# Kernel optimization log

Hardware: AMD Instinct MI355X
Metric: run time of the kernel (lower is better)

The kernel has to match this reference:

```python
import jax, jax.numpy as jnp
import numpy as np

B, T, D_MODEL = 2, 1024, 1024
H, DEPTH = 8, 5
DH = D_MODEL // H


def setup_inputs() -> dict:
    key = jax.random.key(0)
    k_x, k_wp, k_bp, k_wv, k_wo = jax.random.split(key, 5)
    x = jax.random.normal(k_x, (B, T, D_MODEL), dtype=jnp.float32)
    # Parameters stored as [in, out] (y = x @ W + b), equivalent math to nn.Linear.
    Wp = jax.random.normal(k_wp, (D_MODEL, H * DEPTH), dtype=jnp.float32) * 0.02
    bp = jnp.zeros((H * DEPTH,), dtype=jnp.float32)
    Wv = jax.random.normal(k_wv, (D_MODEL, D_MODEL), dtype=jnp.float32) * 0.02
    Wo = jax.random.normal(k_wo, (D_MODEL, D_MODEL), dtype=jnp.float32) * 0.02
    return {"x": x, "Wp": Wp, "bp": bp, "Wv": Wv, "Wo": Wo}


def reference(x, Wp, bp, Wv, Wo):
    Bx, Tx, d = x.shape
    # soft binary path decisions: B,H,T,DEPTH
    paths = jax.nn.sigmoid(x @ Wp + bp)              # B,T,H*DEPTH
    paths = paths.reshape(Bx, Tx, H, DEPTH).transpose(0, 2, 1, 3)  # B,H,T,DEPTH
    # pairwise per-level agreement: B,H,Tq,Tk,DEPTH
    pq = paths[:, :, :, None, :]
    pk = paths[:, :, None, :, :]
    agree = pq * pk + (1.0 - pq) * (1.0 - pk)
    # shared-prefix length via cumprod over depth, summed
    sim = jnp.cumprod(agree, axis=-1).sum(axis=-1) / DEPTH  # B,H,Tq,Tk
    # causal mask
    mask = jnp.triu(jnp.ones((Tx, Tx), dtype=bool), k=1)
    sim = jnp.where(mask[None, None], -jnp.inf, sim)
    attn = jax.nn.softmax(sim, axis=-1)              # B,H,T,T
    V = (x @ Wv).reshape(Bx, Tx, H, DH).transpose(0, 2, 1, 3)  # B,H,T,dh
    ctx = jnp.einsum('bhqk,bhkd->bhqd', attn, V)
    ctx = ctx.transpose(0, 2, 1, 3).reshape(Bx, Tx, d)
    return ctx @ Wo
```

## Files before the change

### kernel.cpp

```cpp
#include <hip/hip_runtime.h>
#include <hip/hip_bf16.h>

#define B_ 2
#define T_ 1024
#define D_ 1024
#define H_ 8
#define DEPTH_ 5
#define DH_ 128

typedef short s16x8 __attribute__((ext_vector_type(8)));
typedef short s16x4 __attribute__((ext_vector_type(4)));
typedef float f32x4 __attribute__((ext_vector_type(4)));

__device__ inline short f2bf(float f) {
  __hip_bfloat16 h = __float2bfloat16(f);
  return *reinterpret_cast<short*>(&h);
}

#define MFMA16(a, b, c) __builtin_amdgcn_mfma_f32_16x16x32_bf16(a, b, c, 0, 0, 0)

typedef __attribute__((address_space(3))) unsigned int lds_u32_t;
typedef __attribute__((address_space(1))) unsigned int glb_u32_t;
__device__ __forceinline__ void glds16(const void* g, void* l) {
  __builtin_amdgcn_global_load_lds((const glb_u32_t*)g, (lds_u32_t*)l, 16, 0,
                                   0);
}

__global__ __launch_bounds__(256) void prep_kernel(
    const float* __restrict__ Wv, const float* __restrict__ Wo,
    const float* __restrict__ Wp, const float* __restrict__ x,
    short* __restrict__ WBt, short* __restrict__ Wot,
    short* __restrict__ xb) {
  int tid = threadIdx.x;
  if (blockIdx.z < 2) {
    const float* W = blockIdx.z ? Wo : Wv;
    short* Wt = blockIdx.z ? Wot : WBt;
    __shared__ float tile[64][65];
    int k0 = blockIdx.y * 64, n0 = blockIdx.x * 64;
#pragma unroll
    for (int i = 0; i < 4; ++i) {
      int idx = tid + i * 256;
      int r = idx >> 4, c4 = (idx & 15) * 4;
      float4 v = *(const float4*)&W[(size_t)(k0 + r) * D_ + n0 + c4];
      tile[r][c4 + 0] = v.x;
      tile[r][c4 + 1] = v.y;
      tile[r][c4 + 2] = v.z;
      tile[r][c4 + 3] = v.w;
    }
    __syncthreads();
#pragma unroll
    for (int j = 0; j < 2; ++j) {
      int idx = tid + j * 256;
      int n = idx >> 3, k8 = (idx & 7) * 8;
      s16x8 outv;
#pragma unroll
      for (int jj = 0; jj < 8; ++jj) outv[jj] = f2bf(tile[k8 + jj][n]);
      *(s16x8*)&Wt[(size_t)(n0 + n) * D_ + k0 + k8] = outv;
    }
  } else {
    int bid = blockIdx.y * 16 + blockIdx.x;
#pragma unroll
    for (int c = 0; c < 4; ++c) {
      size_t idx = (size_t)bid * 8192 + c * 2048 + tid * 8;
      float4 f0 = *(const float4*)&x[idx];
      float4 f1 = *(const float4*)&x[idx + 4];
      s16x8 v;
      v[0] = f2bf(f0.x); v[1] = f2bf(f0.y);
      v[2] = f2bf(f0.z); v[3] = f2bf(f0.w);
      v[4] = f2bf(f1.x); v[5] = f2bf(f1.y);
      v[6] = f2bf(f1.z); v[7] = f2bf(f1.w);
      *(s16x8*)&xb[idx] = v;
    }
    if (bid < 4) {
#pragma unroll
      for (int it = 0; it < 8; ++it) {
        int item = bid * 2048 + it * 256 + tid;
        int row = item >> 7, k8 = (item & 127) * 8;
        s16x8 v;
        if (row < H_ * DEPTH_) {
#pragma unroll
          for (int j = 0; j < 8; ++j)
            v[j] = f2bf(Wp[(size_t)(k8 + j) * (H_ * DEPTH_) + row]);
        } else {
#pragma unroll
          for (int j = 0; j < 8; ++j) v[j] = 0;
        }
        *(s16x8*)&WBt[(size_t)(1024 + row) * D_ + k8] = v;
      }
    }
  }
}

template <int MODE>
__global__ __launch_bounds__(256) void gemm128(
    const short* __restrict__ A, const short* __restrict__ Bt,
    float* __restrict__ Cf, short* __restrict__ Vt,
    const float* __restrict__ bp, float* __restrict__ paths_t) {
  __shared__ short As[64 * 128];
  __shared__ short Bs[64 * 128];
  const int K = D_;
  int tid = threadIdx.x;
  int bm = blockIdx.y << 6, bn = blockIdx.x << 6;
  int w = tid >> 6, lane = tid & 63;
  int wm = (w >> 1) * 32, wn = (w & 1) * 32;
  int g = lane >> 4, fr = lane & 15;
  f32x4 acc[2][2] = {{{0.f, 0.f, 0.f, 0.f}, {0.f, 0.f, 0.f, 0.f}},
                     {{0.f, 0.f, 0.f, 0.f}, {0.f, 0.f, 0.f, 0.f}}};

  int r4 = lane >> 4;
  int cg = lane & 15;
  const short* Asrc[4];
  const short* Bsrc[4];
  short* Adst[4];
  short* Bdst[4];
#pragma unroll
  for (int i = 0; i < 4; ++i) {
    int row = w * 16 + i * 4 + r4;
    int scol = (cg ^ (row & 15)) * 8;
    Asrc[i] = A + (size_t)(bm + row) * K + scol;
    Bsrc[i] = Bt + (size_t)(bn + row) * K + scol;
    Adst[i] = &As[(w * 16 + i * 4) * 128];
    Bdst[i] = &Bs[(w * 16 + i * 4) * 128];
  }

  for (int k0 = 0; k0 < K; k0 += 128) {
    __syncthreads();
#pragma unroll
    for (int i = 0; i < 4; ++i) {
      glds16(Asrc[i] + k0, Adst[i]);
      glds16(Bsrc[i] + k0, Bdst[i]);
    }
    __syncthreads();
#pragma unroll
    for (int ks = 0; ks < 4; ++ks) {
      int p = ((ks * 4 + g) ^ fr) * 8;
      s16x8 a0 = *(const s16x8*)&As[(wm + fr) * 128 + p];
      s16x8 a1 = *(const s16x8*)&As[(wm + 16 + fr) * 128 + p];
      s16x8 b0 = *(const s16x8*)&Bs[(wn + fr) * 128 + p];
      s16x8 b1 = *(const s16x8*)&Bs[(wn + 16 + fr) * 128 + p];
      acc[0][0] = MFMA16(a0, b0, acc[0][0]);
      acc[0][1] = MFMA16(a0, b1, acc[0][1]);
      acc[1][0] = MFMA16(a1, b0, acc[1][0]);
      acc[1][1] = MFMA16(a1, b1, acc[1][1]);
    }
  }
  int col = lane & 15, rbase = (lane >> 4) * 4;
  if (MODE == 0) {
#pragma unroll
    for (int mi = 0; mi < 2; ++mi)
#pragma unroll
      for (int ni = 0; ni < 2; ++ni)
#pragma unroll
        for (int r = 0; r < 4; ++r)
          Cf[(size_t)(bm + wm + mi * 16 + rbase + r) * D_ + bn + wn +
             ni * 16 + col] = acc[mi][ni][r];
  } else if (bn < 1024) {
#pragma unroll
    for (int mi = 0; mi < 2; ++mi)
#pragma unroll
      for (int ni = 0; ni < 2; ++ni) {
        int m = bm + wm + mi * 16 + rbase;
        int n = bn + wn + ni * 16 + col;
        int b = m >> 10, t = m & (T_ - 1);
        int h = n >> 7, dh = n & (DH_ - 1);
        s16x4 v4;
#pragma unroll
        for (int r = 0; r < 4; ++r) v4[r] = f2bf(acc[mi][ni][r]);
        *(s16x4*)&Vt[((size_t)((b * H_ + h) * DH_ + dh)) * T_ + t] = v4;
      }
  } else {
#pragma unroll
    for (int ni = 0; ni < 2; ++ni) {
      int pn = wn + ni * 16 + col;
      if (pn < H_ * DEPTH_) {
        float bias = bp[pn];
        int h = pn / DEPTH_, d = pn % DEPTH_;
#pragma unroll
        for (int mi = 0; mi < 2; ++mi)
#pragma unroll
          for (int r = 0; r < 4; ++r) {
            int m = bm + wm + mi * 16 + rbase + r;
            int b = m >> 10, t = m & (T_ - 1);
            float pv = 1.f / (1.f + __expf(-(acc[mi][ni][r] + bias)));
            paths_t[(((size_t)(b * H_ + h) * T_ + t) * DEPTH_) + d] = pv;
          }
      }
    }
  }
}

#define LS2 136

__global__ __launch_bounds__(512) void attn_kernel(
    const float* __restrict__ paths_t, const short* __restrict__ Vt,
    short* __restrict__ ctxb) {
  int bh = blockIdx.y;
  int b = bh >> 3, h = bh & 7;
  int bx = blockIdx.x;
  int w = threadIdx.x >> 6, lane = threadIdx.x & 63;
  int g = lane >> 4, fr = lane & 15;

  __shared__ short Vs[DH_ * 128];
  __shared__ short Ss[32 * LS2];
  __shared__ float lsum_s[32];

  const float* pb = paths_t + (size_t)bh * T_ * DEPTH_;
  const short* vb = Vt + (size_t)bh * DH_ * T_;

  int r4 = lane >> 4, cg = lane & 15;
  const short* Vsrc[4];
  short* Vdst[4];
#pragma unroll
  for (int i = 0; i < 4; ++i) {
    int row = w * 16 + i * 4 + r4;
    int scol = (cg ^ (row & 15)) * 8;
    Vsrc[i] = vb + (size_t)row * T_ + scol;
    Vdst[i] = &Vs[(w * 16 + i * 4) * 128];
  }

  for (int half = 0; half < 2; ++half) {
    int qt = half ? (31 - bx) : bx;
    int q0 = qt * 32;
    int nkt = (qt >> 2) + 1;

    float pq[4][DEPTH_], mq[4][DEPTH_];
#pragma unroll
    for (int j = 0; j < 4; ++j) {
      const float* qr = pb + (size_t)(q0 + w * 4 + j) * DEPTH_;
#pragma unroll
      for (int d = 0; d < DEPTH_; ++d) {
        pq[j][d] = qr[d];
        mq[j][d] = 1.f - pq[j][d];
      }
    }
    f32x4 acc[2] = {{0.f, 0.f, 0.f, 0.f}, {0.f, 0.f, 0.f, 0.f}};
    float part[4] = {};

    for (int kt = 0; kt < nkt; ++kt) {
      int k0 = kt * 128;
      __syncthreads();
      int kA = k0 + lane, kB = k0 + 64 + lane;
      const float* krA = pb + (size_t)kA * DEPTH_;
      const float* krB = pb + (size_t)kB * DEPTH_;
      float pkA[DEPTH_], mkA[DEPTH_], pkB[DEPTH_], mkB[DEPTH_];
#pragma unroll
      for (int d = 0; d < DEPTH_; ++d) {
        pkA[d] = krA[d];
        pkB[d] = krB[d];
      }
#pragma unroll
      for (int i = 0; i < 4; ++i) glds16(Vsrc[i] + k0, Vdst[i]);
#pragma unroll
      for (int d = 0; d < DEPTH_; ++d) {
        mkA[d] = 1.f - pkA[d];
        mkB[d] = 1.f - pkB[d];
      }
#pragma unroll
      for (int j = 0; j < 4; ++j) {
        int qg = q0 + w * 4 + j;
        {
          float a0 = fmaf(pq[j][0], pkA[0], mq[j][0] * mkA[0]);
          float a1 = fmaf(pq[j][1], pkA[1], mq[j][1] * mkA[1]);
          float a2 = fmaf(pq[j][2], pkA[2], mq[j][2] * mkA[2]);
          float a3 = fmaf(pq[j][3], pkA[3], mq[j][3] * mkA[3]);
          float a4 = fmaf(pq[j][4], pkA[4], mq[j][4] * mkA[4]);
          float t4 = 1.f + a4;
          float t3 = fmaf(a3, t4, 1.f);
          float t2 = fmaf(a2, t3, 1.f);
          float t1 = fmaf(a1, t2, 1.f);
          float s = a0 * t1;
          float wv = (kA <= qg) ? __expf(s * 0.2f) : 0.f;
          part[j] += wv;
          Ss[(w * 4 + j) * LS2 + lane] = f2bf(wv);
        }
        {
          float a0 = fmaf(pq[j][0], pkB[0], mq[j][0] * mkB[0]);
          float a1 = fmaf(pq[j][1], pkB[1], mq[j][1] * mkB[1]);
          float a2 = fmaf(pq[j][2], pkB[2], mq[j][2] * mkB[2]);
          float a3 = fmaf(pq[j][3], pkB[3], mq[j][3] * mkB[3]);
          float a4 = fmaf(pq[j][4], pkB[4], mq[j][4] * mkB[4]);
          float t4 = 1.f + a4;
          float t3 = fmaf(a3, t4, 1.f);
          float t2 = fmaf(a2, t3, 1.f);
          float t1 = fmaf(a1, t2, 1.f);
          float s = a0 * t1;
          float wv = (kB <= qg) ? __expf(s * 0.2f) : 0.f;
          part[j] += wv;
          Ss[(w * 4 + j) * LS2 + 64 + lane] = f2bf(wv);
        }
      }
      __syncthreads();
#pragma unroll
      for (int ks = 0; ks < 4; ++ks) {
        int ko = ks * 32 + g * 8;
        int sl = ((ks * 4 + g) ^ fr) * 8;
        s16x8 sa0 = *(const s16x8*)&Ss[fr * LS2 + ko];
        s16x8 sa1 = *(const s16x8*)&Ss[(16 + fr) * LS2 + ko];
        s16x8 vv = *(const s16x8*)&Vs[(w * 16 + fr) * 128 + sl];
        acc[0] = MFMA16(sa0, vv, acc[0]);
        acc[1] = MFMA16(sa1, vv, acc[1]);
      }
    }
#pragma unroll
    for (int j = 0; j < 4; ++j) {
      float s = part[j];
#pragma unroll
      for (int off = 32; off >= 1; off >>= 1) s += __shfl_xor(s, off, 64);
      if (lane == j) lsum_s[w * 4 + j] = s;
    }
    __syncthreads();
    int col = fr, rbase = g * 4;
#pragma unroll
    for (int qt2 = 0; qt2 < 2; ++qt2)
#pragma unroll
      for (int r = 0; r < 4; ++r) {
        int ql = qt2 * 16 + rbase + r;
        int dh = w * 16 + col;
        float val = acc[qt2][r] / lsum_s[ql];
        ctxb[(size_t)(b * T_ + q0 + ql) * D_ + h * DH_ + dh] = f2bf(val);
      }
    __syncthreads();
  }
}

extern "C" void kernel_launch(void* const* d_in, const int* in_sizes, int n_in,
                              void* d_out, int out_size, void* d_ws,
                              size_t ws_size, hipStream_t stream) {
  const float* x = (const float*)d_in[0];
  const float* Wp = (const float*)d_in[1];
  const float* bp = (const float*)d_in[2];
  const float* Wv = (const float*)d_in[3];
  const float* Wo = (const float*)d_in[4];
  float* out = (float*)d_out;

  char* ws = (char*)d_ws;
  float* paths_t = (float*)ws;
  short* Vt = (short*)(ws + 327680);
  short* WBt = (short*)(ws + 4521984);
  short* Wot = (short*)(ws + 6750208);
  short* ctxb = (short*)(ws + 8847360);
  short* xb = (short*)(ws + 13041664);

  prep_kernel<<<dim3(16, 16, 3), 256, 0, stream>>>(Wv, Wo, Wp, x, WBt, Wot,
                                                   xb);
  gemm128<1><<<dim3(17, 32), 256, 0, stream>>>(xb, WBt, nullptr, Vt, bp,
                                               paths_t);
  attn_kernel<<<dim3(16, B_ * H_), 512, 0, stream>>>(paths_t, Vt, ctxb);
  gemm128<0><<<dim3(16, 32), 256, 0, stream>>>(ctxb, Wot, out, nullptr,
                                               nullptr, nullptr);
}
```

Baseline: 123.0 us.

## Load GEMM MFMA operands directly from global memory instead of LDS staging

Both GEMMs stop staging A and B tiles through shared memory with global_load_lds and barriers. Each lane now loads its MFMA fragments straight from global memory, with the K loop unrolled by 8. This removes LDS traffic and the two barriers per K step. The cost is no operand reuse across waves: each row is fetched by two waves, which doubles global/L2 traffic, and the per-lane 16-byte loads have poorer coalescing.

New measurement: 178.3 us. 1.45x slower.

```diff
diff --git a/kernel.cpp b/kernel.cpp
--- a/kernel.cpp
+++ b/kernel.cpp
@@ -92,58 +92,37 @@
 }
 
 template <int MODE>
-__global__ __launch_bounds__(256) void gemm128(
+__global__ __launch_bounds__(256) void gemm_direct(
     const short* __restrict__ A, const short* __restrict__ Bt,
     float* __restrict__ Cf, short* __restrict__ Vt,
     const float* __restrict__ bp, float* __restrict__ paths_t) {
-  __shared__ short As[64 * 128];
-  __shared__ short Bs[64 * 128];
   const int K = D_;
   int tid = threadIdx.x;
   int bm = blockIdx.y << 6, bn = blockIdx.x << 6;
   int w = tid >> 6, lane = tid & 63;
   int wm = (w >> 1) * 32, wn = (w & 1) * 32;
   int g = lane >> 4, fr = lane & 15;
+
+  const short* Ar0 = A + (size_t)(bm + wm + fr) * K + g * 8;
+  const short* Ar1 = A + (size_t)(bm + wm + 16 + fr) * K + g * 8;
+  const short* Br0 = Bt + (size_t)(bn + wn + fr) * K + g * 8;
+  const short* Br1 = Bt + (size_t)(bn + wn + 16 + fr) * K + g * 8;
+
   f32x4 acc[2][2] = {{{0.f, 0.f, 0.f, 0.f}, {0.f, 0.f, 0.f, 0.f}},
                      {{0.f, 0.f, 0.f, 0.f}, {0.f, 0.f, 0.f, 0.f}}};
 
-  int r4 = lane >> 4;
-  int cg = lane & 15;
-  const short* Asrc[4];
-  const short* Bsrc[4];
-  short* Adst[4];
-  short* Bdst[4];
-#pragma unroll
-  for (int i = 0; i < 4; ++i) {
-    int row = w * 16 + i * 4 + r4;
-    int scol = (cg ^ (row & 15)) * 8;
-    Asrc[i] = A + (size_t)(bm + row) * K + scol;
-    Bsrc[i] = Bt + (size_t)(bn + row) * K + scol;
-    Adst[i] = &As[(w * 16 + i * 4) * 128];
-    Bdst[i] = &Bs[(w * 16 + i * 4) * 128];
-  }
-
-  for (int k0 = 0; k0 < K; k0 += 128) {
-    __syncthreads();
-#pragma unroll
-    for (int i = 0; i < 4; ++i) {
-      glds16(Asrc[i] + k0, Adst[i]);
-      glds16(Bsrc[i] + k0, Bdst[i]);
-    }
-    __syncthreads();
-#pragma unroll
-    for (int ks = 0; ks < 4; ++ks) {
-      int p = ((ks * 4 + g) ^ fr) * 8;
-      s16x8 a0 = *(const s16x8*)&As[(wm + fr) * 128 + p];
-      s16x8 a1 = *(const s16x8*)&As[(wm + 16 + fr) * 128 + p];
-      s16x8 b0 = *(const s16x8*)&Bs[(wn + fr) * 128 + p];
-      s16x8 b1 = *(const s16x8*)&Bs[(wn + 16 + fr) * 128 + p];
-      acc[0][0] = MFMA16(a0, b0, acc[0][0]);
-      acc[0][1] = MFMA16(a0, b1, acc[0][1]);
-      acc[1][0] = MFMA16(a1, b0, acc[1][0]);
-      acc[1][1] = MFMA16(a1, b1, acc[1][1]);
-    }
-  }
+#pragma unroll 8
+  for (int k0 = 0; k0 < K; k0 += 32) {
+    s16x8 a0 = *(const s16x8*)(Ar0 + k0);
+    s16x8 a1 = *(const s16x8*)(Ar1 + k0);
+    s16x8 b0 = *(const s16x8*)(Br0 + k0);
+    s16x8 b1 = *(const s16x8*)(Br1 + k0);
+    acc[0][0] = MFMA16(a0, b0, acc[0][0]);
+    acc[0][1] = MFMA16(a0, b1, acc[0][1]);
+    acc[1][0] = MFMA16(a1, b0, acc[1][0]);
+    acc[1][1] = MFMA16(a1, b1, acc[1][1]);
+  }
+
   int col = lane & 15, rbase = (lane >> 4) * 4;
   if (MODE == 0) {
 #pragma unroll
@@ -343,9 +322,9 @@
 
   prep_kernel<<<dim3(16, 16, 3), 256, 0, stream>>>(Wv, Wo, Wp, x, WBt, Wot,
                                                    xb);
-  gemm128<1><<<dim3(17, 32), 256, 0, stream>>>(xb, WBt, nullptr, Vt, bp,
-                                               paths_t);
+  gemm_direct<1><<<dim3(17, 32), 256, 0, stream>>>(xb, WBt, nullptr, Vt, bp,
+                                                   paths_t);
   attn_kernel<<<dim3(16, B_ * H_), 512, 0, stream>>>(paths_t, Vt, ctxb);
-  gemm128<0><<<dim3(16, 32), 256, 0, stream>>>(ctxb, Wot, out, nullptr,
-                                               nullptr, nullptr);
-}
+  gemm_direct<0><<<dim3(16, 32), 256, 0, stream>>>(ctxb, Wot, out, nullptr,
+                                                   nullptr, nullptr);
+}
```
